# Performance work log

Hardware: AMD Instinct MI355X
Metric: run time of the kernel (lower is better)

## Reference

```python
import jax, jax.numpy as jnp
import numpy as np

L = 4            # n_layers
D_MODEL = 768
D_STATE = 16
D_CONV = 4
EXPAND = 2
D_INNER = EXPAND * D_MODEL      # 1536
DT_RANK = (D_MODEL + 15) // 16  # 48
B = 2
T = 2048
LN_EPS = 1e-5


def setup_inputs() -> dict:
    key = jax.random.key(0)
    ks = jax.random.split(key, 12)
    s = 0.02
    x = jax.random.normal(ks[0], (B, T, D_MODEL), dtype=jnp.float32)
    in_proj_w = jax.random.normal(ks[1], (L, 2 * D_INNER, D_MODEL), dtype=jnp.float32) * s
    conv_w = jax.random.normal(ks[2], (L, D_INNER, D_CONV), dtype=jnp.float32) * s
    conv_b = jnp.zeros((L, D_INNER), dtype=jnp.float32)
    x_proj_w = jax.random.normal(ks[3], (L, DT_RANK + 2 * D_STATE, D_INNER), dtype=jnp.float32) * s
    dt_proj_w = jax.random.normal(ks[4], (L, D_INNER, DT_RANK), dtype=jnp.float32) * s
    dt_proj_b = jax.random.normal(ks[5], (L, D_INNER), dtype=jnp.float32) * 0.1
    # Standard S4D-real init: A = -[1..d_state], stored as log
    A_log = jnp.log(jnp.broadcast_to(
        jnp.arange(1, D_STATE + 1, dtype=jnp.float32), (L, D_INNER, D_STATE)))
    D_param = jnp.ones((L, D_INNER), dtype=jnp.float32)
    out_proj_w = jax.random.normal(ks[6], (L, D_MODEL, D_INNER), dtype=jnp.float32) * s
    ln_g = jnp.ones((L, D_MODEL), dtype=jnp.float32)
    ln_b = jnp.zeros((L, D_MODEL), dtype=jnp.float32)
    return {"x": x, "in_proj_w": in_proj_w, "conv_w": conv_w, "conv_b": conv_b,
            "x_proj_w": x_proj_w, "dt_proj_w": dt_proj_w, "dt_proj_b": dt_proj_b,
            "A_log": A_log, "D_param": D_param, "out_proj_w": out_proj_w,
            "ln_g": ln_g, "ln_b": ln_b}


def _layernorm(x, g, b):
    mu = jnp.mean(x, axis=-1, keepdims=True)
    var = jnp.mean(jnp.square(x - mu), axis=-1, keepdims=True)
    return (x - mu) * jax.lax.rsqrt(var + LN_EPS) * g + b


def _mamba_layer(x, inw, convw, convb, xpw, dtw, dtb, A_log, Dp, outw):
    # x: [B,T,d_model]
    Tn = x.shape[1]
    xz = jnp.einsum('btd,ed->bte', x, inw)          # [B,T,2*d_inner]
    xin, z = jnp.split(xz, 2, axis=-1)              # each [B,T,d_inner]
    # causal depthwise conv1d over time (kernel d_conv)
    xp = jnp.pad(xin, ((0, 0), (D_CONV - 1, 0), (0, 0)))
    xc = convb
    for k in range(D_CONV):
        xc = xc + xp[:, k:k + Tn, :] * convw[:, k]
    xc = jax.nn.silu(xc)                            # [B,T,d_inner]
    dbl = jnp.einsum('bti,ei->bte', xc, xpw)        # [B,T,dt_rank+2*d_state]
    dt, Bs, Cs = jnp.split(dbl, [DT_RANK, DT_RANK + D_STATE], axis=-1)
    dt = jax.nn.softplus(jnp.einsum('btr,dr->btd', dt, dtw) + dtb)  # [B,T,d_inner]
    A = -jnp.exp(A_log)                             # [d_inner,d_state]
    dA = jnp.exp(jnp.einsum('btd,dn->btdn', dt, A))  # discretized A
    dBu = (dt * xc)[..., None] * Bs[:, :, None, :]   # [B,T,d_inner,d_state]

    def step(h, inp):
        dA_t, dBu_t, C_t = inp                      # [B,d,n],[B,d,n],[B,n]
        h = dA_t * h + dBu_t
        y = jnp.einsum('bdn,bn->bd', h, C_t)
        return h, y

    h0 = jnp.zeros((x.shape[0], D_INNER, D_STATE), x.dtype)
    _, ys = jax.lax.scan(step, h0,
                         (jnp.swapaxes(dA, 0, 1), jnp.swapaxes(dBu, 0, 1),
                          jnp.swapaxes(Cs, 0, 1)))
    y = jnp.swapaxes(ys, 0, 1) + xc * Dp            # skip connection D*u
    y = y * jax.nn.silu(z)                          # gate
    return jnp.einsum('bti,ei->bte', y, outw)       # [B,T,d_model]


def reference(x, in_proj_w, conv_w, conv_b, x_proj_w, dt_proj_w, dt_proj_b,
              A_log, D_param, out_proj_w, ln_g, ln_b):
    for l in range(L):
        residual = x
        h = _mamba_layer(x, in_proj_w[l], conv_w[l], conv_b[l], x_proj_w[l],
                         dt_proj_w[l], dt_proj_b[l], A_log[l], D_param[l],
                         out_proj_w[l])
        h = _layernorm(h, ln_g[l], ln_b[l])
        x = h + residual                            # dropout=0 -> identity
    return x
```

## Files before the change

### kernel.cpp

```cpp
#include <hip/hip_runtime.h>

#define T_LEN 2048
#define DM    768
#define DI    1536
#define DS    16
#define BB    2
#define NROWS (BB * T_LEN)
#define NCH   128
#define CLEN  16
#define NSEG  8
#define SEGC  16

#define OFF_DTB 0
#define OFF_A   6144
#define OFF_DP  104448
#define OFF_CW  110592
#define OFF_CB  135168
#define OFF_LG  141312
#define OFF_LB  144384
#define PRM_TOT 147456

typedef __attribute__((ext_vector_type(8))) short bh8;
typedef __attribute__((ext_vector_type(4))) float f32x4;

typedef const __attribute__((address_space(1))) void as1_void;
typedef __attribute__((address_space(3))) void as3_void;

__device__ __forceinline__ void glds16(const void* g, void* l) {
    __builtin_amdgcn_global_load_lds((as1_void*)g, (as3_void*)l, 16, 0, 0);
}

__device__ __forceinline__ float bf2f(unsigned short u) {
    return __uint_as_float(((unsigned)u) << 16);
}
__device__ __forceinline__ unsigned short f2bf(float f) {
    unsigned u = __float_as_uint(f);
    u += 0x7FFFu + ((u >> 16) & 1u);
    return (unsigned short)(u >> 16);
}
__device__ __forceinline__ float ldin(const void* p, long i, int bf) {
    return bf ? bf2f(((const unsigned short*)p)[i]) : ((const float*)p)[i];
}

__global__ void k_sniff(const unsigned short* __restrict__ x, int* __restrict__ flag) {
    __shared__ int cnt[4];
    int tid = threadIdx.x;
    int local = 0;
#pragma unroll
    for (int j = 0; j < 4; ++j) {
        unsigned short u = x[tid * 4 + j];
        int e = (u >> 7) & 0xFF;
        if (e >= 100 && e <= 140) local++;
    }
    for (int off = 32; off; off >>= 1) local += __shfl_down(local, off, 64);
    if ((tid & 63) == 0) cnt[tid >> 6] = local;
    __syncthreads();
    if (tid == 0) {
        int tot = cnt[0] + cnt[1] + cnt[2] + cnt[3];
        *flag = (tot >= 900) ? 1 : 0;
    }
}

__global__ void k_prep(const void* in_x, const void* in_inw, const void* in_ow,
                       const void* in_xpw, const void* in_dtw,
                       const void* dtb, const void* alog, const void* dpar,
                       const void* cw, const void* cb, const void* lg, const void* lb,
                       unsigned short* __restrict__ xbf, float* __restrict__ xf,
                       unsigned short* __restrict__ Win, unsigned short* __restrict__ Wout,
                       unsigned short* __restrict__ Wxp, unsigned short* __restrict__ Wdt,
                       float* __restrict__ prm, const int* __restrict__ flag) {
    const long E0 = 3145728L;
    const long E1 = E0 + 9437184L;
    const long E2 = E1 + 4718592L;
    const long E3 = E2 + 786432L;
    const long E4 = E3 + 393216L;
    const long E5 = E4 + 147456L;
    int bf = *flag;
    long gid = (long)blockIdx.x * 256 + threadIdx.x;
    if (gid < E0) {
        float v = ldin(in_x, gid, bf);
        xbf[gid] = f2bf(v);
        xf[gid]  = v;
    } else if (gid < E1) {
        long i = gid - E0;
        Win[i] = bf ? ((const unsigned short*)in_inw)[i] : f2bf(((const float*)in_inw)[i]);
    } else if (gid < E2) {
        long i = gid - E1;
        Wout[i] = bf ? ((const unsigned short*)in_ow)[i] : f2bf(((const float*)in_ow)[i]);
    } else if (gid < E3) {
        long i = gid - E2;
        int c = (int)(i % 1536);
        long rl = i / 1536;
        int r = (int)(rl % 128);
        int l = (int)(rl / 128);
        unsigned short v = 0;
        if (r < 80) {
            long si = ((long)l * 80 + r) * 1536 + c;
            v = bf ? ((const unsigned short*)in_xpw)[si] : f2bf(((const float*)in_xpw)[si]);
        }
        Wxp[i] = v;
    } else if (gid < E4) {
        long i = gid - E3;
        int c = (int)(i % 64);
        long rl = i / 64;
        int d = (int)(rl % 1536);
        int l = (int)(rl / 1536);
        unsigned short v = 0;
        if (c < 48) {
            long si = ((long)l * 1536 + d) * 48 + c;
            v = bf ? ((const unsigned short*)in_dtw)[si] : f2bf(((const float*)in_dtw)[si]);
        }
        Wdt[i] = v;
    } else if (gid < E5) {
        int i = (int)(gid - E4);
        float v;
        if (i < OFF_A)        v = ldin(dtb, i - OFF_DTB, bf);
        else if (i < OFF_DP)  v = -__expf(ldin(alog, i - OFF_A, bf));
        else if (i < OFF_CW)  v = ldin(dpar, i - OFF_DP, bf);
        else if (i < OFF_CB)  v = ldin(cw, i - OFF_CW, bf);
        else if (i < OFF_LG)  v = ldin(cb, i - OFF_CB, bf);
        else if (i < OFF_LB)  v = ldin(lg, i - OFF_LG, bf);
        else                  v = ldin(lb, i - OFF_LB, bf);
        prm[i] = v;
    }
}

__global__ __launch_bounds__(256) void k_gemm128(const unsigned short* __restrict__ A,
                                                 const unsigned short* __restrict__ B,
                                                 unsigned short* __restrict__ C,
                                                 int M, int N, int K) {
    __shared__ __align__(16) unsigned short As[128 * 32];
    __shared__ __align__(16) unsigned short Bs[128 * 32];
    const int tid = threadIdx.x;
    const int lane = tid & 63, wid = tid >> 6;
    const int wm = wid >> 1, wn = wid & 1;
    const long arow0 = (long)blockIdx.y * 128;
    const long bcol0 = (long)blockIdx.x * 128;
    const int r16 = lane >> 2;
    const int c8  = (lane & 3) * 8;
    f32x4 acc[4][4] = {};

    for (int k0 = 0; k0 < K; k0 += 32) {
#pragma unroll
        for (int j = 0; j < 2; ++j) {
            int chunk = wid + j * 4;
            int row = chunk * 16 + r16;
            glds16(&A[(arow0 + row) * K + k0 + c8], &As[chunk * 512]);
            glds16(&B[(bcol0 + row) * K + k0 + c8], &Bs[chunk * 512]);
        }
        __syncthreads();
        const int row = lane & 15, q8 = (lane >> 4) * 8;
        bh8 af[4], bfr[4];
#pragma unroll
        for (int i = 0; i < 4; ++i) af[i] = *(const bh8*)&As[(wm * 64 + i * 16 + row) * 32 + q8];
#pragma unroll
        for (int i = 0; i < 4; ++i) bfr[i] = *(const bh8*)&Bs[(wn * 64 + i * 16 + row) * 32 + q8];
#pragma unroll
        for (int i = 0; i < 4; ++i)
#pragma unroll
            for (int j = 0; j < 4; ++j)
                acc[i][j] = __builtin_amdgcn_mfma_f32_16x16x32_bf16(af[i], bfr[j], acc[i][j], 0, 0, 0);
        __syncthreads();
    }
    const int crow = (lane >> 4) * 4, ccol = lane & 15;
#pragma unroll
    for (int i = 0; i < 4; ++i)
#pragma unroll
        for (int j = 0; j < 4; ++j)
#pragma unroll
            for (int r = 0; r < 4; ++r) {
                long gr = arow0 + wm * 64 + i * 16 + crow + r;
                long gc = bcol0 + wn * 64 + j * 16 + ccol;
                C[gr * N + gc] = f2bf(acc[i][j][r]);
            }
}

__global__ __launch_bounds__(256) void k_xproj(const unsigned short* __restrict__ A,
                                               const unsigned short* __restrict__ B,
                                               float* __restrict__ C) {
    __shared__ __align__(16) unsigned short As[64 * 32];
    __shared__ __align__(16) unsigned short Bs[64 * 32];
    const int tid = threadIdx.x;
    const int lane = tid & 63, wid = tid >> 6;
    const int wm = wid >> 1, wn = wid & 1;
    const long arow0 = (long)blockIdx.y * 64;
    const long bcol0 = (long)blockIdx.x * 64;
    const int kbase = blockIdx.z * 384;
    const int r16 = lane >> 2;
    const int c8  = (lane & 3) * 8;
    f32x4 acc[2][2] = {};

    for (int kk = 0; kk < 384; kk += 32) {
        int k0 = kbase + kk;
        int row = wid * 16 + r16;
        glds16(&A[(arow0 + row) * DI + k0 + c8], &As[wid * 512]);
        glds16(&B[(bcol0 + row) * DI + k0 + c8], &Bs[wid * 512]);
        __syncthreads();
        const int row2 = lane & 15, q8 = (lane >> 4) * 8;
        bh8 af[2], bfr[2];
#pragma unroll
        for (int i = 0; i < 2; ++i) af[i] = *(const bh8*)&As[(wm * 32 + i * 16 + row2) * 32 + q8];
#pragma unroll
        for (int i = 0; i < 2; ++i) bfr[i] = *(const bh8*)&Bs[(wn * 32 + i * 16 + row2) * 32 + q8];
#pragma unroll
        for (int i = 0; i < 2; ++i)
#pragma unroll
            for (int j = 0; j < 2; ++j)
                acc[i][j] = __builtin_amdgcn_mfma_f32_16x16x32_bf16(af[i], bfr[j], acc[i][j], 0, 0, 0);
        __syncthreads();
    }
    const int crow = (lane >> 4) * 4, ccol = lane & 15;
#pragma unroll
    for (int i = 0; i < 2; ++i)
#pragma unroll
        for (int j = 0; j < 2; ++j)
#pragma unroll
            for (int r = 0; r < 4; ++r) {
                long gr = arow0 + wm * 32 + i * 16 + crow + r;
                long gc = bcol0 + wn * 32 + j * 16 + ccol;
                atomicAdd(&C[gr * 128 + gc], acc[i][j][r]);
            }
}

__global__ __launch_bounds__(256) void k_dtproj(const float* __restrict__ Dbl,
                                                const unsigned short* __restrict__ Wdt,
                                                const float* __restrict__ bias,
                                                unsigned short* __restrict__ Dt) {
    __shared__ __align__(16) unsigned short As[2 * 64 * 32];
    __shared__ __align__(16) unsigned short Bs[2 * 64 * 32];
    const int tid = threadIdx.x;
    const int lane = tid & 63, wid = tid >> 6;
    const int wm = wid >> 1, wn = wid & 1;
    const long arow0 = (long)blockIdx.y * 64;
    const long bcol0 = (long)blockIdx.x * 64;

    {
        int r = tid >> 2;
        int cs = (tid & 3) * 16;
        unsigned short tmp[16];
#pragma unroll
        for (int q = 0; q < 4; ++q) {
            int col0 = cs + q * 4;
            if (col0 < 48) {
                f32x4 v = *(const f32x4*)&Dbl[(arow0 + r) * 128 + col0];
#pragma unroll
                for (int j = 0; j < 4; ++j) tmp[q * 4 + j] = f2bf(v[j]);
            } else {
#pragma unroll
                for (int j = 0; j < 4; ++j) tmp[q * 4 + j] = 0;
            }
        }
        int p = cs >> 5;
        int cp = cs & 31;
        *(bh8*)&As[p * 2048 + r * 32 + cp]     = *(bh8*)&tmp[0];
        *(bh8*)&As[p * 2048 + r * 32 + cp + 8] = *(bh8*)&tmp[8];
    }
#pragma unroll
    for (int j = 0; j < 2; ++j) {
        int chunk = tid + j * 256;
        int p = chunk >> 8;
        int rem = chunk & 255;
        int row = rem >> 2;
        int c4 = rem & 3;
        glds16(&Wdt[(bcol0 + row) * 64 + p * 32 + c4 * 8], &Bs[chunk * 8]);
    }
    __syncthreads();

    const int row2 = lane & 15, q8 = (lane >> 4) * 8;
    f32x4 acc[2][2] = {};
#pragma unroll
    for (int p = 0; p < 2; ++p) {
        bh8 af[2], bfr[2];
#pragma unroll
        for (int i = 0; i < 2; ++i) af[i] = *(const bh8*)&As[p * 2048 + (wm * 32 + i * 16 + row2) * 32 + q8];
#pragma unroll
        for (int i = 0; i < 2; ++i) bfr[i] = *(const bh8*)&Bs[p * 2048 + (wn * 32 + i * 16 + row2) * 32 + q8];
#pragma unroll
        for (int i = 0; i < 2; ++i)
#pragma unroll
            for (int j = 0; j < 2; ++j)
                acc[i][j] = __builtin_amdgcn_mfma_f32_16x16x32_bf16(af[i], bfr[j], acc[i][j], 0, 0, 0);
    }
    const int crow = (lane >> 4) * 4, ccol = lane & 15;
#pragma unroll
    for (int i = 0; i < 2; ++i)
#pragma unroll
        for (int j = 0; j < 2; ++j)
#pragma unroll
            for (int r = 0; r < 4; ++r) {
                long gr = arow0 + wm * 32 + i * 16 + crow + r;
                long gc = bcol0 + wn * 32 + j * 16 + ccol;
                float v = acc[i][j][r] + bias[gc];
                v = (v > 20.f) ? v : log1pf(__expf(v));
                Dt[gr * DI + gc] = f2bf(v);
            }
}

__global__ __launch_bounds__(256) void k_outproj(const unsigned short* __restrict__ A,
                                                 const unsigned short* __restrict__ B,
                                                 float* __restrict__ C) {
    __shared__ __align__(16) unsigned short As[64 * 32];
    __shared__ __align__(16) unsigned short Bs[64 * 32];
    const int tid = threadIdx.x;
    const int lane = tid & 63, wid = tid >> 6;
    const int wm = wid >> 1, wn = wid & 1;
    const long arow0 = (long)blockIdx.y * 64;
    const long bcol0 = (long)blockIdx.x * 64;
    const int r16 = lane >> 2;
    const int c8  = (lane & 3) * 8;
    f32x4 acc[2][2] = {};

    for (int k0 = 0; k0 < DI; k0 += 32) {
        int row = wid * 16 + r16;
        glds16(&A[(arow0 + row) * DI + k0 + c8], &As[wid * 512]);
        glds16(&B[(bcol0 + row) * DI + k0 + c8], &Bs[wid * 512]);
        __syncthreads();
        const int row2 = lane & 15, q8 = (lane >> 4) * 8;
        bh8 af[2], bfr[2];
#pragma unroll
        for (int i = 0; i < 2; ++i) af[i] = *(const bh8*)&As[(wm * 32 + i * 16 + row2) * 32 + q8];
#pragma unroll
        for (int i = 0; i < 2; ++i) bfr[i] = *(const bh8*)&Bs[(wn * 32 + i * 16 + row2) * 32 + q8];
#pragma unroll
        for (int i = 0; i < 2; ++i)
#pragma unroll
            for (int j = 0; j < 2; ++j)
                acc[i][j] = __builtin_amdgcn_mfma_f32_16x16x32_bf16(af[i], bfr[j], acc[i][j], 0, 0, 0);
        __syncthreads();
    }
    const int crow = (lane >> 4) * 4, ccol = lane & 15;
#pragma unroll
    for (int i = 0; i < 2; ++i)
#pragma unroll
        for (int j = 0; j < 2; ++j)
#pragma unroll
            for (int r = 0; r < 4; ++r) {
                long gr = arow0 + wm * 32 + i * 16 + crow + r;
                long gc = bcol0 + wn * 32 + j * 16 + ccol;
                C[gr * DM + gc] = acc[i][j][r];
            }
}

__global__ __launch_bounds__(256) void k_conv(const unsigned short* __restrict__ xz,
                                              const float* __restrict__ cw,
                                              const float* __restrict__ cb,
                                              unsigned short* __restrict__ xcbf) {
    __shared__ float tile[131 * 64];
    const int tid = threadIdx.x;
    const int d0 = blockIdx.x * 64;
    const long t0 = (long)blockIdx.y * 128;
    const bool seqstart = ((int)t0 & (T_LEN - 1)) == 0;
    for (int j = tid; j < 131 * 64; j += 256) {
        int row = j >> 6, col = j & 63;
        float v = 0.f;
        if (!(seqstart && row < 3)) v = bf2f(xz[(t0 - 3 + row) * (2 * DI) + d0 + col]);
        tile[j] = v;
    }
    __syncthreads();
    const int d = tid & 63, tl0 = tid >> 6;
    const int dg = d0 + d;
    const float w0 = cw[dg * 4 + 0], w1 = cw[dg * 4 + 1];
    const float w2 = cw[dg * 4 + 2], w3 = cw[dg * 4 + 3];
    const float bias = cb[dg];
    for (int tt = tl0; tt < 128; tt += 4) {
        float acc = bias + w0 * tile[tt * 64 + d] + w1 * tile[(tt + 1) * 64 + d]
                         + w2 * tile[(tt + 2) * 64 + d] + w3 * tile[(tt + 3) * 64 + d];
        float s = acc / (1.f + __expf(-acc));
        xcbf[(t0 + tt) * DI + dg] = f2bf(s);
    }
}

__global__ __launch_bounds__(256) void k_scan1(const unsigned short* __restrict__ dt,
                                               const unsigned short* __restrict__ xcbf,
                                               const float* __restrict__ dbl,
                                               const float* __restrict__ An,
                                               float* __restrict__ hch,
                                               float* __restrict__ sdtb) {
    const int tid = threadIdx.x;
    const int db = blockIdx.x % 6;
    const int c  = (blockIdx.x / 6) % NCH;
    const int b  = blockIdx.x / (6 * NCH);
    const int d  = db * 256 + tid;
    const int t0 = c * CLEN;
    float h[DS], An_r[DS];
    const f32x4* Ap = (const f32x4*)(An + (long)d * DS);
#pragma unroll
    for (int q = 0; q < 4; ++q) {
        f32x4 a4 = Ap[q];
#pragma unroll
        for (int j = 0; j < 4; ++j) { An_r[q * 4 + j] = a4[j]; h[q * 4 + j] = 0.f; }
    }
    float sdt = 0.f;
    const long rowb = (long)b * T_LEN + t0;
#pragma unroll 4
    for (int s = 0; s < CLEN; ++s) {
        long bt = rowb + s;
        float dtv = bf2f(dt[bt * DI + d]);
        float xcv = bf2f(xcbf[bt * DI + d]);
        int bi = __builtin_amdgcn_readfirstlane((int)(bt * 128 + 48));
        const f32x4* bp = (const f32x4*)(dbl + bi);
        float Bv[DS];
#pragma unroll
        for (int q = 0; q < 4; ++q) {
            f32x4 b4 = bp[q];
#pragma unroll
            for (int j = 0; j < 4; ++j) Bv[q * 4 + j] = b4[j];
        }
        float du = dtv * xcv;
        sdt += dtv;
#pragma unroll
        for (int n = 0; n < DS; ++n)
            h[n] = __expf(An_r[n] * dtv) * h[n] + du * Bv[n];
    }
    long o = (((long)b * NCH + c) * DI + d) * DS;
    f32x4* hp = (f32x4*)(hch + o);
#pragma unroll
    for (int q = 0; q < 4; ++q) {
        f32x4 h4;
#pragma unroll
        for (int j = 0; j < 4; ++j) h4[j] = h[q * 4 + j];
        hp[q] = h4;
    }
    sdtb[((long)b * NCH + c) * DI + d] = sdt;
}

__global__ __launch_bounds__(256) void k_scan2a(float* __restrict__ hbuf,
                                                const float* __restrict__ sdtb,
                                                const float* __restrict__ An,
                                                float* __restrict__ cum,
                                                float* __restrict__ Gseg,
                                                float* __restrict__ Sseg) {
    long gid = (long)blockIdx.x * 256 + threadIdx.x;
    int n = (int)(gid & 15);
    long t = gid >> 4;
    int d  = (int)(t % DI);
    int sg = (int)((t / DI) & (NSEG - 1));
    int b  = (int)(t / (DI * NSEG));
    float an = An[(long)d * DS + n];
    float h = 0.f, cs = 0.f;
    for (int i = 0; i < SEGC; ++i) {
        int c = sg * SEGC + i;
        long rowi = ((long)b * NCH + c) * DI + d;
        long idx = rowi * DS + n;
        float sdt = sdtb[rowi];
        float g = hbuf[idx];
        hbuf[idx] = h;
        if (n == 0) cum[rowi] = cs;
        h = __expf(an * sdt) * h + g;
        cs += sdt;
    }
    long gi = (((long)b * NSEG + sg) * DI + d) * DS + n;
    Gseg[gi] = h;
    if (n == 0) Sseg[((long)b * NSEG + sg) * DI + d] = cs;
}

__global__ __launch_bounds__(256) void k_scan2b(const float* __restrict__ Gseg,
                                                const float* __restrict__ Sseg,
                                                const float* __restrict__ An,
                                                float* __restrict__ Hseg) {
    long gid = (long)blockIdx.x * 256 + threadIdx.x;
    int n = (int)(gid & 15);
    long t = gid >> 4;
    int d = (int)(t % DI);
    int b = (int)(t / DI);
    float an = An[(long)d * DS + n];
    float H = 0.f;
    for (int sg = 0; sg < NSEG; ++sg) {
        long gi = (((long)b * NSEG + sg) * DI + d) * DS + n;
        float G = Gseg[gi];
        float S = Sseg[((long)b * NSEG + sg) * DI + d];
        Hseg[gi] = H;
        H = __expf(an * S) * H + G;
    }
}

__global__ __launch_bounds__(256) void k_scan3(const unsigned short* __restrict__ dt,
                                               const unsigned short* __restrict__ xcbf,
                                               const float* __restrict__ dbl,
                                               const float* __restrict__ An,
                                               const float* __restrict__ Dp,
                                               const float* __restrict__ hpref,
                                               const float* __restrict__ cum,
                                               const float* __restrict__ Hseg,
                                               const unsigned short* __restrict__ xz,
                                               unsigned short* __restrict__ ybf) {
    const int tid = threadIdx.x;
    const int db = blockIdx.x % 6;
    const int c  = (blockIdx.x / 6) % NCH;
    const int b  = blockIdx.x / (6 * NCH);
    const int d  = db * 256 + tid;
    const int t0 = c * CLEN;
    const int sg = c / SEGC;
    float h[DS], An_r[DS];
    long rowi = ((long)b * NCH + c) * DI + d;
    long o = rowi * DS;
    long gi = (((long)b * NSEG + sg) * DI + d) * DS;
    const float cs = cum[rowi];
    const f32x4* Ap = (const f32x4*)(An + (long)d * DS);
    const f32x4* Pp = (const f32x4*)(hpref + o);
    const f32x4* Hp = (const f32x4*)(Hseg + gi);
#pragma unroll
    for (int q = 0; q < 4; ++q) {
        f32x4 a4 = Ap[q], p4 = Pp[q], h4 = Hp[q];
#pragma unroll
        for (int j = 0; j < 4; ++j) {
            int n = q * 4 + j;
            An_r[n] = a4[j];
            h[n] = __expf(a4[j] * cs) * h4[j] + p4[j];
        }
    }
    const float dcoef = Dp[d];
    const long rowb = (long)b * T_LEN + t0;
#pragma unroll 4
    for (int s = 0; s < CLEN; ++s) {
        long bt = rowb + s;
        float dtv = bf2f(dt[bt * DI + d]);
        float xcv = bf2f(xcbf[bt * DI + d]);
        int bi = __builtin_amdgcn_readfirstlane((int)(bt * 128 + 48));
        const f32x4* bp = (const f32x4*)(dbl + bi);
        float Bv[DS], Cv[DS];
#pragma unroll
        for (int q = 0; q < 4; ++q) {
            f32x4 b4 = bp[q], c4 = bp[q + 4];
#pragma unroll
            for (int j = 0; j < 4; ++j) { Bv[q * 4 + j] = b4[j]; Cv[q * 4 + j] = c4[j]; }
        }
        float du = dtv * xcv;
        float yp[4] = {xcv * dcoef, 0.f, 0.f, 0.f};
#pragma unroll
        for (int n = 0; n < DS; ++n) {
            h[n] = __expf(An_r[n] * dtv) * h[n] + du * Bv[n];
            yp[n & 3] += h[n] * Cv[n];
        }
        float y = (yp[0] + yp[1]) + (yp[2] + yp[3]);
        float zv = bf2f(xz[bt * (2 * DI) + DI + d]);
        y *= zv / (1.f + __expf(-zv));
        ybf[bt * DI + d] = f2bf(y);
    }
}

__global__ __launch_bounds__(256) void k_ln(const float* __restrict__ prj,
                                            float* __restrict__ x,
                                            unsigned short* __restrict__ xbf,
                                            const float* __restrict__ lg,
                                            const float* __restrict__ lb,
                                            void* __restrict__ dout,
                                            int is_last, const int* __restrict__ flag) {
    __shared__ float red[8];
    const int row = blockIdx.x;
    const int tid = threadIdx.x;
    float v[3];
    float s = 0.f, s2 = 0.f;
#pragma unroll
    for (int j = 0; j < 3; ++j) {
        v[j] = prj[(long)row * DM + tid + j * 256];
        s += v[j];
        s2 += v[j] * v[j];
    }
    for (int off = 32; off; off >>= 1) {
        s  += __shfl_down(s, off, 64);
        s2 += __shfl_down(s2, off, 64);
    }
    if ((tid & 63) == 0) { red[tid >> 6] = s; red[4 + (tid >> 6)] = s2; }
    __syncthreads();
    float S  = red[0] + red[1] + red[2] + red[3];
    float S2 = red[4] + red[5] + red[6] + red[7];
    float mu = S * (1.f / DM);
    float var = S2 * (1.f / DM) - mu * mu;
    float rs = rsqrtf(var + 1e-5f);
    int bf = *flag;
#pragma unroll
    for (int j = 0; j < 3; ++j) {
        int e = tid + j * 256;
        long idx = (long)row * DM + e;
        float out = (v[j] - mu) * rs * lg[e] + lb[e] + x[idx];
        x[idx] = out;
        xbf[idx] = f2bf(out);
        if (is_last) {
            if (bf) ((unsigned short*)dout)[idx] = f2bf(out);
            else    ((float*)dout)[idx] = out;
        }
    }
}

extern "C" void kernel_launch(void* const* d_in, const int* in_sizes, int n_in,
                              void* d_out, int out_size, void* d_ws, size_t ws_size,
                              hipStream_t stream) {
    char* ws = (char*)d_ws;
    const size_t O_FLAG = 0;
    const size_t O_WIN  = 256;
    const size_t O_WXP  = O_WIN  + 18874368;
    const size_t O_WDT  = O_WXP  + 1572864;
    const size_t O_WOUT = O_WDT  + 786432;
    const size_t O_PRM  = O_WOUT + 9437184;
    const size_t O_XBF  = O_PRM  + 589824;
    const size_t O_XF   = O_XBF  + 6291456;
    const size_t O_XZ   = O_XF   + 12582912;
    const size_t O_XCBF = O_XZ   + 25165824;
    const size_t O_DBL  = O_XCBF + 12582912;
    const size_t O_DT   = O_DBL  + 2097152;
    const size_t O_HCH  = O_DT   + 12582912;
    const size_t O_SDT  = O_HCH  + 25165824;
    const size_t O_CUM  = O_SDT  + 1572864;
    const size_t O_GSEG = O_CUM  + 1572864;
    const size_t O_SSEG = O_GSEG + 1572864;
    const size_t O_HSEG = O_SSEG + 98304;
    const size_t O_YBF  = O_HSEG + 1572864;

    int* flag = (int*)(ws + O_FLAG);
    unsigned short* Win  = (unsigned short*)(ws + O_WIN);
    unsigned short* Wxp  = (unsigned short*)(ws + O_WXP);
    unsigned short* Wdt  = (unsigned short*)(ws + O_WDT);
    unsigned short* Wout = (unsigned short*)(ws + O_WOUT);
    float* prm = (float*)(ws + O_PRM);
    unsigned short* Xbf = (unsigned short*)(ws + O_XBF);
    float* Xf  = (float*)(ws + O_XF);
    unsigned short* Xz = (unsigned short*)(ws + O_XZ);
    unsigned short* Xcbf = (unsigned short*)(ws + O_XCBF);
    float* Dbl = (float*)(ws + O_DBL);
    unsigned short* Dt = (unsigned short*)(ws + O_DT);
    float* Hch = (float*)(ws + O_HCH);
    float* Sdt = (float*)(ws + O_SDT);
    float* Cum = (float*)(ws + O_CUM);
    float* Gsg = (float*)(ws + O_GSEG);
    float* Ssg = (float*)(ws + O_SSEG);
    float* Hsg = (float*)(ws + O_HSEG);
    unsigned short* Ybf = (unsigned short*)(ws + O_YBF);
    float* Prj = (float*)(ws + O_XZ);

    k_sniff<<<1, 256, 0, stream>>>((const unsigned short*)d_in[0], flag);
    k_prep<<<72768, 256, 0, stream>>>(d_in[0], d_in[1], d_in[9], d_in[4], d_in[5],
                                      d_in[6], d_in[7], d_in[8], d_in[2], d_in[3],
                                      d_in[10], d_in[11],
                                      Xbf, Xf, Win, Wout, Wxp, Wdt, prm, flag);

    for (int l = 0; l < 4; ++l) {
        const unsigned short* winL  = Win  + (size_t)l * 3072 * 768;
        const unsigned short* wxpL  = Wxp  + (size_t)l * 128 * 1536;
        const unsigned short* wdtL  = Wdt  + (size_t)l * 1536 * 64;
        const unsigned short* woutL = Wout + (size_t)l * 768 * 1536;
        const float* cwL  = prm + OFF_CW  + (size_t)l * DI * 4;
        const float* cbL  = prm + OFF_CB  + (size_t)l * DI;
        const float* dtbL = prm + OFF_DTB + (size_t)l * DI;
        const float* anL  = prm + OFF_A   + (size_t)l * DI * DS;
        const float* dpL  = prm + OFF_DP  + (size_t)l * DI;
        const float* lgL  = prm + OFF_LG  + (size_t)l * DM;
        const float* lbL  = prm + OFF_LB  + (size_t)l * DM;

        k_gemm128<<<dim3(24, 32), 256, 0, stream>>>(Xbf, winL, Xz, NROWS, 2 * DI, DM);
        k_conv<<<dim3(24, 32), 256, 0, stream>>>(Xz, cwL, cbL, Xcbf);
        hipMemsetAsync(Dbl, 0, 2097152, stream);
        k_xproj<<<dim3(2, 64, 4), 256, 0, stream>>>(Xcbf, wxpL, Dbl);
        k_dtproj<<<dim3(24, 64), 256, 0, stream>>>(Dbl, wdtL, dtbL, Dt);
        k_scan1<<<BB * NCH * 6, 256, 0, stream>>>(Dt, Xcbf, Dbl, anL, Hch, Sdt);
        k_scan2a<<<1536, 256, 0, stream>>>(Hch, Sdt, anL, Cum, Gsg, Ssg);
        k_scan2b<<<192, 256, 0, stream>>>(Gsg, Ssg, anL, Hsg);
        k_scan3<<<BB * NCH * 6, 256, 0, stream>>>(Dt, Xcbf, Dbl, anL, dpL, Hch, Cum, Hsg, Xz, Ybf);
        k_outproj<<<dim3(12, 64), 256, 0, stream>>>(Ybf, woutL, Prj);
        k_ln<<<4096, 256, 0, stream>>>(Prj, Xf, Xbf, lgL, lbL, d_out, (l == 3) ? 1 : 0, flag);
    }
}
```

Before: 912.0 us.

## Vectorize prep, drop xproj split-K atomics, reuse 128-tile GEMM for outproj, resize scan chunks

The prep kernel now handles 8 elements per thread with vector loads and stores, so it launches far fewer blocks. The x_proj GEMM no longer splits K across blocks with atomicAdd; it uses 32-row tiles over the full K, which also removes the memset of its output. The out_proj GEMM switches to the templated 128x128 GEMM that writes fp32. The scan is regrouped into 64 chunks of length 32 with 8 chunks per segment, and the workspace sizes are shrunk to match. The out_proj change yields only 192 blocks, which may leave many compute units idle.

```diff
diff --git a/kernel.cpp b/kernel.cpp
--- a/kernel.cpp
+++ b/kernel.cpp
@@ -6,10 +6,10 @@
 #define DS    16
 #define BB    2
 #define NROWS (BB * T_LEN)
-#define NCH   128
-#define CLEN  16
+#define NCH   64
+#define CLEN  32
 #define NSEG  8
-#define SEGC  16
+#define SEGC  8
 
 #define OFF_DTB 0
 #define OFF_A   6144
@@ -38,8 +38,32 @@
     u += 0x7FFFu + ((u >> 16) & 1u);
     return (unsigned short)(u >> 16);
 }
-__device__ __forceinline__ float ldin(const void* p, long i, int bf) {
-    return bf ? bf2f(((const unsigned short*)p)[i]) : ((const float*)p)[i];
+
+__device__ __forceinline__ void ld8(const void* p, long e0, int bf, float* v) {
+    if (bf) {
+        bh8 u = *(const bh8*)((const unsigned short*)p + e0);
+#pragma unroll
+        for (int j = 0; j < 8; ++j) v[j] = bf2f((unsigned short)u[j]);
+    } else {
+        const f32x4* q = (const f32x4*)((const float*)p + e0);
+        f32x4 a = q[0], b = q[1];
+#pragma unroll
+        for (int j = 0; j < 4; ++j) { v[j] = a[j]; v[4 + j] = b[j]; }
+    }
+}
+
+__device__ __forceinline__ void cp8(unsigned short* dst, long de0,
+                                    const void* src, long se0, int bf) {
+    if (bf) {
+        *(bh8*)&dst[de0] = *(const bh8*)((const unsigned short*)src + se0);
+    } else {
+        const f32x4* q = (const f32x4*)((const float*)src + se0);
+        f32x4 a = q[0], b = q[1];
+        bh8 o;
+#pragma unroll
+        for (int j = 0; j < 4; ++j) { o[j] = (short)f2bf(a[j]); o[4 + j] = (short)f2bf(b[j]); }
+        *(bh8*)&dst[de0] = o;
+    }
 }
 
 __global__ void k_sniff(const unsigned short* __restrict__ x, int* __restrict__ flag) {
@@ -69,65 +93,76 @@
                        unsigned short* __restrict__ Win, unsigned short* __restrict__ Wout,
                        unsigned short* __restrict__ Wxp, unsigned short* __restrict__ Wdt,
                        float* __restrict__ prm, const int* __restrict__ flag) {
-    const long E0 = 3145728L;
-    const long E1 = E0 + 9437184L;
-    const long E2 = E1 + 4718592L;
-    const long E3 = E2 + 786432L;
-    const long E4 = E3 + 393216L;
-    const long E5 = E4 + 147456L;
+    const long G0 = 393216L;
+    const long G1 = G0 + 1179648L;
+    const long G2 = G1 + 589824L;
+    const long G3 = G2 + 98304L;
+    const long G4 = G3 + 49152L;
+    const long G5 = G4 + 18432L;
     int bf = *flag;
-    long gid = (long)blockIdx.x * 256 + threadIdx.x;
-    if (gid < E0) {
-        float v = ldin(in_x, gid, bf);
-        xbf[gid] = f2bf(v);
-        xf[gid]  = v;
-    } else if (gid < E1) {
-        long i = gid - E0;
-        Win[i] = bf ? ((const unsigned short*)in_inw)[i] : f2bf(((const float*)in_inw)[i]);
-    } else if (gid < E2) {
-        long i = gid - E1;
-        Wout[i] = bf ? ((const unsigned short*)in_ow)[i] : f2bf(((const float*)in_ow)[i]);
-    } else if (gid < E3) {
-        long i = gid - E2;
-        int c = (int)(i % 1536);
-        long rl = i / 1536;
+    long g = (long)blockIdx.x * 256 + threadIdx.x;
+    if (g >= G5) return;
+    if (g < G0) {
+        long e0 = g * 8;
+        float v[8];
+        ld8(in_x, e0, bf, v);
+        bh8 o;
+#pragma unroll
+        for (int j = 0; j < 8; ++j) o[j] = (short)f2bf(v[j]);
+        *(bh8*)&xbf[e0] = o;
+        f32x4 a, b;
+#pragma unroll
+        for (int j = 0; j < 4; ++j) { a[j] = v[j]; b[j] = v[4 + j]; }
+        ((f32x4*)&xf[e0])[0] = a;
+        ((f32x4*)&xf[e0])[1] = b;
+    } else if (g < G1) {
+        long e0 = (g - G0) * 8;
+        cp8(Win, e0, in_inw, e0, bf);
+    } else if (g < G2) {
+        long e0 = (g - G1) * 8;
+        cp8(Wout, e0, in_ow, e0, bf);
+    } else if (g < G3) {
+        long e0 = (g - G2) * 8;
+        int c = (int)(e0 % 1536);
+        long rl = e0 / 1536;
         int r = (int)(rl % 128);
         int l = (int)(rl / 128);
-        unsigned short v = 0;
-        if (r < 80) {
-            long si = ((long)l * 80 + r) * 1536 + c;
-            v = bf ? ((const unsigned short*)in_xpw)[si] : f2bf(((const float*)in_xpw)[si]);
-        }
-        Wxp[i] = v;
-    } else if (gid < E4) {
-        long i = gid - E3;
-        int c = (int)(i % 64);
-        long rl = i / 64;
+        if (r < 80) cp8(Wxp, e0, in_xpw, ((long)l * 80 + r) * 1536 + c, bf);
+        else        *(bh8*)&Wxp[e0] = (bh8)(short)0;
+    } else if (g < G4) {
+        long e0 = (g - G3) * 8;
+        int c = (int)(e0 & 63);
+        long rl = e0 >> 6;
         int d = (int)(rl % 1536);
         int l = (int)(rl / 1536);
-        unsigned short v = 0;
-        if (c < 48) {
-            long si = ((long)l * 1536 + d) * 48 + c;
-            v = bf ? ((const unsigned short*)in_dtw)[si] : f2bf(((const float*)in_dtw)[si]);
-        }
-        Wdt[i] = v;
-    } else if (gid < E5) {
-        int i = (int)(gid - E4);
-        float v;
-        if (i < OFF_A)        v = ldin(dtb, i - OFF_DTB, bf);
-        else if (i < OFF_DP)  v = -__expf(ldin(alog, i - OFF_A, bf));
-        else if (i < OFF_CW)  v = ldin(dpar, i - OFF_DP, bf);
-        else if (i < OFF_CB)  v = ldin(cw, i - OFF_CW, bf);
-        else if (i < OFF_LG)  v = ldin(cb, i - OFF_CB, bf);
-        else if (i < OFF_LB)  v = ldin(lg, i - OFF_LG, bf);
-        else                  v = ldin(lb, i - OFF_LB, bf);
-        prm[i] = v;
-    }
-}
-
+        if (c < 48) cp8(Wdt, e0, in_dtw, ((long)l * 1536 + d) * 48 + c, bf);
+        else        *(bh8*)&Wdt[e0] = (bh8)(short)0;
+    } else {
+        long e0 = (g - G4) * 8;
+        float v[8];
+        if (e0 < OFF_A)        ld8(dtb,  e0 - OFF_DTB, bf, v);
+        else if (e0 < OFF_DP) {
+            ld8(alog, e0 - OFF_A, bf, v);
+#pragma unroll
+            for (int j = 0; j < 8; ++j) v[j] = -__expf(v[j]);
+        }
+        else if (e0 < OFF_CW)  ld8(dpar, e0 - OFF_DP, bf, v);
+        else if (e0 < OFF_CB)  ld8(cw,   e0 - OFF_CW, bf, v);
+        else if (e0 < OFF_LG)  ld8(cb,   e0 - OFF_CB, bf, v);
+        else if (e0 < OFF_LB)  ld8(lg,   e0 - OFF_LG, bf, v);
+        else                   ld8(lb,   e0 - OFF_LB, bf, v);
+        f32x4 a, b;
+#pragma unroll
+        for (int j = 0; j < 4; ++j) { a[j] = v[j]; b[j] = v[4 + j]; }
+        ((f32x4*)&prm[e0])[0] = a;
+        ((f32x4*)&prm[e0])[1] = b;
+    }
+}
+
+template <int OUTF32>
 __global__ __launch_bounds__(256) void k_gemm128(const unsigned short* __restrict__ A,
                                                  const unsigned short* __restrict__ B,
-                                                 unsigned short* __restrict__ C,
+                                                 void* __restrict__ Cv,
                                                  int M, int N, int K) {
     __shared__ __align__(16) unsigned short As[128 * 32];
     __shared__ __align__(16) unsigned short Bs[128 * 32];
@@ -171,55 +206,50 @@
             for (int r = 0; r < 4; ++r) {
                 long gr = arow0 + wm * 64 + i * 16 + crow + r;
                 long gc = bcol0 + wn * 64 + j * 16 + ccol;
-                C[gr * N + gc] = f2bf(acc[i][j][r]);
+                if (OUTF32) ((float*)Cv)[gr * N + gc] = acc[i][j][r];
+                else ((unsigned short*)Cv)[gr * N + gc] = f2bf(acc[i][j][r]);
             }
 }
 
 __global__ __launch_bounds__(256) void k_xproj(const unsigned short* __restrict__ A,
                                                const unsigned short* __restrict__ B,
                                                float* __restrict__ C) {
-    __shared__ __align__(16) unsigned short As[64 * 32];
+    __shared__ __align__(16) unsigned short As[32 * 32];
     __shared__ __align__(16) unsigned short Bs[64 * 32];
     const int tid = threadIdx.x;
-    const int lane = tid & 63, wid = tid >> 6;
-    const int wm = wid >> 1, wn = wid & 1;
-    const long arow0 = (long)blockIdx.y * 64;
+    const int lane = tid & 63, w = tid >> 6;
+    const int wm = w >> 1, wn = w & 1;
+    const long arow0 = (long)blockIdx.y * 32;
     const long bcol0 = (long)blockIdx.x * 64;
-    const int kbase = blockIdx.z * 384;
-    const int r16 = lane >> 2;
-    const int c8  = (lane & 3) * 8;
-    f32x4 acc[2][2] = {};
-
-    for (int kk = 0; kk < 384; kk += 32) {
-        int k0 = kbase + kk;
-        int row = wid * 16 + r16;
-        glds16(&A[(arow0 + row) * DI + k0 + c8], &As[wid * 512]);
-        glds16(&B[(bcol0 + row) * DI + k0 + c8], &Bs[wid * 512]);
+    const int r4 = lane >> 2;
+    const int c8 = (lane & 3) * 8;
+    f32x4 acc[2] = {};
+
+    for (int k0 = 0; k0 < DI; k0 += 32) {
+        if (w < 2) {
+            glds16(&A[(arow0 + w * 16 + r4) * DI + k0 + c8], &As[w * 512]);
+            glds16(&B[(bcol0 + 32 + w * 16 + r4) * DI + k0 + c8], &Bs[1024 + w * 512]);
+        } else {
+            glds16(&B[(bcol0 + (w - 2) * 16 + r4) * DI + k0 + c8], &Bs[(w - 2) * 512]);
+        }
         __syncthreads();
         const int row2 = lane & 15, q8 = (lane >> 4) * 8;
-        bh8 af[2], bfr[2];
-#pragma unroll
-        for (int i = 0; i < 2; ++i) af[i] = *(const bh8*)&As[(wm * 32 + i * 16 + row2) * 32 + q8];
-#pragma unroll
-        for (int i = 0; i < 2; ++i) bfr[i] = *(const bh8*)&Bs[(wn * 32 + i * 16 + row2) * 32 + q8];
-#pragma unroll
-        for (int i = 0; i < 2; ++i)
-#pragma unroll
-            for (int j = 0; j < 2; ++j)
-                acc[i][j] = __builtin_amdgcn_mfma_f32_16x16x32_bf16(af[i], bfr[j], acc[i][j], 0, 0, 0);
+        bh8 af = *(const bh8*)&As[(wm * 16 + row2) * 32 + q8];
+        bh8 b0 = *(const bh8*)&Bs[(wn * 32 + row2) * 32 + q8];
+        bh8 b1 = *(const bh8*)&Bs[(wn * 32 + 16 + row2) * 32 + q8];
+        acc[0] = __builtin_amdgcn_mfma_f32_16x16x32_bf16(af, b0, acc[0], 0, 0, 0);
+        acc[1] = __builtin_amdgcn_mfma_f32_16x16x32_bf16(af, b1, acc[1], 0, 0, 0);
         __syncthreads();
     }
     const int crow = (lane >> 4) * 4, ccol = lane & 15;
 #pragma unroll
-    for (int i = 0; i < 2; ++i)
-#pragma unroll
-        for (int j = 0; j < 2; ++j)
-#pragma unroll
-            for (int r = 0; r < 4; ++r) {
-                long gr = arow0 + wm * 32 + i * 16 + crow + r;
-                long gc = bcol0 + wn * 32 + j * 16 + ccol;
-                atomicAdd(&C[gr * 128 + gc], acc[i][j][r]);
-            }
+    for (int j = 0; j < 2; ++j)
+#pragma unroll
+        for (int r = 0; r < 4; ++r) {
+            long gr = arow0 + wm * 16 + crow + r;
+            long gc = bcol0 + wn * 32 + j * 16 + ccol;
+            C[gr * 128 + gc] = acc[j][r];
+        }
 }
 
 __global__ __launch_bounds__(256) void k_dtproj(const float* __restrict__ Dbl,
@@ -293,51 +323,6 @@
                 float v = acc[i][j][r] + bias[gc];
                 v = (v > 20.f) ? v : log1pf(__expf(v));
                 Dt[gr * DI + gc] = f2bf(v);
-            }
-}
-
-__global__ __launch_bounds__(256) void k_outproj(const unsigned short* __restrict__ A,
-                                                 const unsigned short* __restrict__ B,
-                                                 float* __restrict__ C) {
-    __shared__ __align__(16) unsigned short As[64 * 32];
-    __shared__ __align__(16) unsigned short Bs[64 * 32];
-    const int tid = threadIdx.x;
-    const int lane = tid & 63, wid = tid >> 6;
-    const int wm = wid >> 1, wn = wid & 1;
-    const long arow0 = (long)blockIdx.y * 64;
-    const long bcol0 = (long)blockIdx.x * 64;
-    const int r16 = lane >> 2;
-    const int c8  = (lane & 3) * 8;
-    f32x4 acc[2][2] = {};
-
-    for (int k0 = 0; k0 < DI; k0 += 32) {
-        int row = wid * 16 + r16;
-        glds16(&A[(arow0 + row) * DI + k0 + c8], &As[wid * 512]);
-        glds16(&B[(bcol0 + row) * DI + k0 + c8], &Bs[wid * 512]);
-        __syncthreads();
-        const int row2 = lane & 15, q8 = (lane >> 4) * 8;
-        bh8 af[2], bfr[2];
-#pragma unroll
-        for (int i = 0; i < 2; ++i) af[i] = *(const bh8*)&As[(wm * 32 + i * 16 + row2) * 32 + q8];
-#pragma unroll
-        for (int i = 0; i < 2; ++i) bfr[i] = *(const bh8*)&Bs[(wn * 32 + i * 16 + row2) * 32 + q8];
-#pragma unroll
-        for (int i = 0; i < 2; ++i)
-#pragma unroll
-            for (int j = 0; j < 2; ++j)
-                acc[i][j] = __builtin_amdgcn_mfma_f32_16x16x32_bf16(af[i], bfr[j], acc[i][j], 0, 0, 0);
-        __syncthreads();
-    }
-    const int crow = (lane >> 4) * 4, ccol = lane & 15;
-#pragma unroll
-    for (int i = 0; i < 2; ++i)
-#pragma unroll
-        for (int j = 0; j < 2; ++j)
-#pragma unroll
-            for (int r = 0; r < 4; ++r) {
-                long gr = arow0 + wm * 32 + i * 16 + crow + r;
-                long gc = bcol0 + wn * 32 + j * 16 + ccol;
-                C[gr * DM + gc] = acc[i][j][r];
             }
 }
 
@@ -600,9 +585,9 @@
     const size_t O_DBL  = O_XCBF + 12582912;
     const size_t O_DT   = O_DBL  + 2097152;
     const size_t O_HCH  = O_DT   + 12582912;
-    const size_t O_SDT  = O_HCH  + 25165824;
-    const size_t O_CUM  = O_SDT  + 1572864;
-    const size_t O_GSEG = O_CUM  + 1572864;
+    const size_t O_SDT  = O_HCH  + 12582912;
+    const size_t O_CUM  = O_SDT  + 786432;
+    const size_t O_GSEG = O_CUM  + 786432;
     const size_t O_SSEG = O_GSEG + 1572864;
     const size_t O_HSEG = O_SSEG + 98304;
     const size_t O_YBF  = O_HSEG + 1572864;
@@ -629,10 +614,10 @@
     float* Prj = (float*)(ws + O_XZ);
 
     k_sniff<<<1, 256, 0, stream>>>((const unsigned short*)d_in[0], flag);
-    k_prep<<<72768, 256, 0, stream>>>(d_in[0], d_in[1], d_in[9], d_in[4], d_in[5],
-                                      d_in[6], d_in[7], d_in[8], d_in[2], d_in[3],
-                                      d_in[10], d_in[11],
-                                      Xbf, Xf, Win, Wout, Wxp, Wdt, prm, flag);
+    k_prep<<<9096, 256, 0, stream>>>(d_in[0], d_in[1], d_in[9], d_in[4], d_in[5],
+                                     d_in[6], d_in[7], d_in[8], d_in[2], d_in[3],
+                                     d_in[10], d_in[11],
+                                     Xbf, Xf, Win, Wout, Wxp, Wdt, prm, flag);
 
     for (int l = 0; l < 4; ++l) {
         const unsigned short* winL  = Win  + (size_t)l * 3072 * 768;
@@ -647,16 +632,15 @@
         const float* lgL  = prm + OFF_LG  + (size_t)l * DM;
         const float* lbL  = prm + OFF_LB  + (size_t)l * DM;
 
-        k_gemm128<<<dim3(24, 32), 256, 0, stream>>>(Xbf, winL, Xz, NROWS, 2 * DI, DM);
+        k_gemm128<0><<<dim3(24, 32), 256, 0, stream>>>(Xbf, winL, Xz, NROWS, 2 * DI, DM);
         k_conv<<<dim3(24, 32), 256, 0, stream>>>(Xz, cwL, cbL, Xcbf);
-        hipMemsetAsync(Dbl, 0, 2097152, stream);
-        k_xproj<<<dim3(2, 64, 4), 256, 0, stream>>>(Xcbf, wxpL, Dbl);
+        k_xproj<<<dim3(2, 128), 256, 0, stream>>>(Xcbf, wxpL, Dbl);
         k_dtproj<<<dim3(24, 64), 256, 0, stream>>>(Dbl, wdtL, dtbL, Dt);
         k_scan1<<<BB * NCH * 6, 256, 0, stream>>>(Dt, Xcbf, Dbl, anL, Hch, Sdt);
         k_scan2a<<<1536, 256, 0, stream>>>(Hch, Sdt, anL, Cum, Gsg, Ssg);
         k_scan2b<<<192, 256, 0, stream>>>(Gsg, Ssg, anL, Hsg);
         k_scan3<<<BB * NCH * 6, 256, 0, stream>>>(Dt, Xcbf, Dbl, anL, dpL, Hch, Cum, Hsg, Xz, Ybf);
-        k_outproj<<<dim3(12, 64), 256, 0, stream>>>(Ybf, woutL, Prj);
+        k_gemm128<1><<<dim3(6, 32), 256, 0, stream>>>(Ybf, woutL, Prj, NROWS, DM, DI);
         k_ln<<<4096, 256, 0, stream>>>(Prj, Xf, Xbf, lgL, lbL, d_out, (l == 3) ? 1 : 0, flag);
     }
 }
```

Result: slower. 948.9 us (+4.0%).
